# Performance work log

Measured on AMD Instinct MI355X. Metric: run time of the kernel, lower is better.

## Reference

```python
import jax, jax.numpy as jnp
import numpy as np

B, N, T, C = 2, 8192, 32, 64
K, NUM_BASES = 16, 4


def setup_inputs() -> dict:
    key = jax.random.key(0)
    k1, k2, k3, k4, k5 = jax.random.split(key, 5)
    z = jax.random.normal(k1, (B, N, T, C), dtype=jnp.float32)
    neighbor_indices = jax.random.randint(k2, (N, K), 0, N)
    # adjacency initialized as ones + small noise (matches torch init)
    adjacency = jnp.ones((N, K), jnp.float32) + jax.random.normal(k3, (N, K), jnp.float32) * 0.01
    basis_weights = jax.random.normal(k4, (NUM_BASES, N, K), jnp.float32) * 0.02
    channel_coeffs = jax.random.normal(k5, (C, NUM_BASES), jnp.float32)
    return {
        "z": z,
        "neighbor_indices": neighbor_indices,
        "adjacency": adjacency,
        "basis_weights": basis_weights,
        "channel_coeffs": channel_coeffs,
    }


def reference(z, neighbor_indices, adjacency, basis_weights, channel_coeffs):
    # eff_weights: (C, N, K) = einsum over bases ('cb,bnk->cnk' == torch 'ck,knm->cnm')
    eff_weights = jnp.einsum("cb,bnk->cnk", channel_coeffs, basis_weights)
    edge_weights = eff_weights * adjacency[None, :, :]          # (C, N, K)
    z_neigh = z[:, neighbor_indices]                            # (B, N, K, T, C) gather
    # weighted reduction over neighbor axis k, then tanh
    z_out = jnp.einsum("bnktc,cnk->bntc", z_neigh, edge_weights)  # (B, N, T, C)
    return jnp.tanh(z_out)
```

## Files before the change

### kernel.cpp

```cpp
#include <hip/hip_runtime.h>

#define B_ 2
#define N_ 8192
#define T_ 32
#define C_ 64
#define K_ 16
#define NB_ 4

__global__ __launch_bounds__(256) void geodcd_kernel(
    const float* __restrict__ z,
    const int*   __restrict__ nidx,
    const float* __restrict__ adj,
    const float* __restrict__ bw,
    const float* __restrict__ cc,
    float*       __restrict__ out)
{
    const int n   = blockIdx.x;
    const int tid = threadIdx.x;

    __shared__ float ew[K_][C_];
    __shared__ int   idx_s[K_];

    if (tid < K_) idx_s[tid] = nidx[n * K_ + tid];

    for (int i = tid; i < K_ * C_; i += 256) {
        const int k = i >> 6;
        const int c = i & 63;
        float s = 0.f;
#pragma unroll
        for (int b = 0; b < NB_; ++b)
            s += cc[c * NB_ + b] * bw[(b * N_ + n) * K_ + k];
        ew[k][c] = s * adj[n * K_ + k];
    }
    __syncthreads();

    const int c4 = (tid & 15) * 4;
    const int t0 = tid >> 4;

    float4 w[K_];
#pragma unroll
    for (int k = 0; k < K_; ++k)
        w[k] = *(const float4*)&ew[k][c4];

    int zoff[K_];
#pragma unroll
    for (int k = 0; k < K_; ++k)
        zoff[k] = idx_s[k] * (T_ * C_);

#pragma unroll
    for (int b = 0; b < B_; ++b) {
        const float* zb = z   + (size_t)b * (N_ * T_ * C_);
        float*       ob = out + (size_t)b * (N_ * T_ * C_) + n * (T_ * C_);
#pragma unroll
        for (int tt = 0; tt < 2; ++tt) {
            const int t = t0 + tt * 16;
            const int rowoff = t * C_ + c4;
            float4 acc = make_float4(0.f, 0.f, 0.f, 0.f);
#pragma unroll
            for (int k = 0; k < K_; ++k) {
                const float4 v = *(const float4*)&zb[zoff[k] + rowoff];
                acc.x += v.x * w[k].x;
                acc.y += v.y * w[k].y;
                acc.z += v.z * w[k].z;
                acc.w += v.w * w[k].w;
            }
            float4 r;
            r.x = 1.f - 2.f / (__expf(2.f * acc.x) + 1.f);
            r.y = 1.f - 2.f / (__expf(2.f * acc.y) + 1.f);
            r.z = 1.f - 2.f / (__expf(2.f * acc.z) + 1.f);
            r.w = 1.f - 2.f / (__expf(2.f * acc.w) + 1.f);
            *(float4*)&ob[rowoff] = r;
        }
    }
}

extern "C" void kernel_launch(void* const* d_in, const int* in_sizes, int n_in,
                              void* d_out, int out_size, void* d_ws, size_t ws_size,
                              hipStream_t stream) {
    const float* z    = (const float*)d_in[0];
    const int*   nidx = (const int*)  d_in[1];
    const float* adj  = (const float*)d_in[2];
    const float* bw   = (const float*)d_in[3];
    const float* cc   = (const float*)d_in[4];
    float*       out  = (float*)d_out;

    geodcd_kernel<<<N_, 256, 0, stream>>>(z, nidx, adj, bw, cc, out);
}
```

Measured before the change: 491.5 us.

## Retile grid over node groups and (batch, time) slabs with register-computed weights

Each block now handles 16 nodes for one batch and a 2-timestep slab, and the grid's second dimension runs over batch and time chunks. The (C,K) edge weight table is no longer built in shared memory; each thread computes its weights in registers from per-node adj*basis products and the channel coefficients. Stores are nontemporal. The aim is to spread work so that consecutive blocks touch the same time slab of z, improving cache locality for the random gather, and to cut the shared-memory weight setup. The cost is that weight computation is repeated across 32 block rows, and each thread now has fewer loads in flight.

```diff
diff --git a/kernel.cpp b/kernel.cpp
--- a/kernel.cpp
+++ b/kernel.cpp
@@ -7,6 +7,11 @@
 #define K_ 16
 #define NB_ 4
 
+#define NC 16
+#define TC 2
+
+typedef float f4v __attribute__((ext_vector_type(4)));
+
 __global__ __launch_bounds__(256) void geodcd_kernel(
     const float* __restrict__ z,
     const int*   __restrict__ nidx,
@@ -15,63 +20,81 @@
     const float* __restrict__ cc,
     float*       __restrict__ out)
 {
-    const int n   = blockIdx.x;
     const int tid = threadIdx.x;
+    const int n0  = blockIdx.x * NC;
+    const int ph  = blockIdx.y;
+    const int b   = ph >> 4;
+    const int t0  = (ph & 15) * TC;
 
-    __shared__ float ew[K_][C_];
-    __shared__ int   idx_s[K_];
+    __shared__ __align__(16) float qs[NC][K_][NB_];
+    __shared__ int idx_s[NC][K_];
 
-    if (tid < K_) idx_s[tid] = nidx[n * K_ + tid];
-
-    for (int i = tid; i < K_ * C_; i += 256) {
-        const int k = i >> 6;
-        const int c = i & 63;
-        float s = 0.f;
-#pragma unroll
-        for (int b = 0; b < NB_; ++b)
-            s += cc[c * NB_ + b] * bw[(b * N_ + n) * K_ + k];
-        ew[k][c] = s * adj[n * K_ + k];
+    {
+        const int nl = tid >> 4, k = tid & 15;
+        idx_s[nl][k] = nidx[(n0 + nl) * K_ + k];
+    }
+    for (int i = tid; i < NC * K_ * NB_; i += 256) {
+        const int nl = i >> 6;
+        const int k  = (i >> 2) & 15;
+        const int bb = i & 3;
+        qs[nl][k][bb] = adj[(n0 + nl) * K_ + k] * bw[(bb * N_ + (n0 + nl)) * K_ + k];
     }
     __syncthreads();
 
-    const int c4 = (tid & 15) * 4;
-    const int t0 = tid >> 4;
+    const int lane = tid & 15;
+    const int nl   = tid >> 4;
+    const int c4   = lane * 4;
+    const int n    = n0 + nl;
 
-    float4 w[K_];
+    f4v ccv[4];
+#pragma unroll
+    for (int j = 0; j < 4; ++j)
+        ccv[j] = *(const f4v*)&cc[(c4 + j) * NB_];
+
+    f4v w[K_];
+#pragma unroll
+    for (int k = 0; k < K_; ++k) {
+        const f4v q = *(const f4v*)qs[nl][k];
+        f4v wv;
+        wv.x = ccv[0].x * q.x + ccv[0].y * q.y + ccv[0].z * q.z + ccv[0].w * q.w;
+        wv.y = ccv[1].x * q.x + ccv[1].y * q.y + ccv[1].z * q.z + ccv[1].w * q.w;
+        wv.z = ccv[2].x * q.x + ccv[2].y * q.y + ccv[2].z * q.z + ccv[2].w * q.w;
+        wv.w = ccv[3].x * q.x + ccv[3].y * q.y + ccv[3].z * q.z + ccv[3].w * q.w;
+        w[k] = wv;
+    }
+
+    int off[K_];
 #pragma unroll
     for (int k = 0; k < K_; ++k)
-        w[k] = *(const float4*)&ew[k][c4];
+        off[k] = idx_s[nl][k] * (T_ * C_) + t0 * C_ + c4;
 
-    int zoff[K_];
+    const float* zb = z + (size_t)b * (N_ * T_ * C_);
+    f4v a0 = {0.f, 0.f, 0.f, 0.f};
+    f4v a1 = {0.f, 0.f, 0.f, 0.f};
 #pragma unroll
-    for (int k = 0; k < K_; ++k)
-        zoff[k] = idx_s[k] * (T_ * C_);
+    for (int k = 0; k < K_; ++k) {
+        const float* p = zb + off[k];
+        const f4v v0 = *(const f4v*)p;
+        const f4v v1 = *(const f4v*)(p + C_);
+        a0.x += v0.x * w[k].x;  a0.y += v0.y * w[k].y;
+        a0.z += v0.z * w[k].z;  a0.w += v0.w * w[k].w;
+        a1.x += v1.x * w[k].x;  a1.y += v1.y * w[k].y;
+        a1.z += v1.z * w[k].z;  a1.w += v1.w * w[k].w;
+    }
 
-#pragma unroll
-    for (int b = 0; b < B_; ++b) {
-        const float* zb = z   + (size_t)b * (N_ * T_ * C_);
-        float*       ob = out + (size_t)b * (N_ * T_ * C_) + n * (T_ * C_);
-#pragma unroll
-        for (int tt = 0; tt < 2; ++tt) {
-            const int t = t0 + tt * 16;
-            const int rowoff = t * C_ + c4;
-            float4 acc = make_float4(0.f, 0.f, 0.f, 0.f);
-#pragma unroll
-            for (int k = 0; k < K_; ++k) {
-                const float4 v = *(const float4*)&zb[zoff[k] + rowoff];
-                acc.x += v.x * w[k].x;
-                acc.y += v.y * w[k].y;
-                acc.z += v.z * w[k].z;
-                acc.w += v.w * w[k].w;
-            }
-            float4 r;
-            r.x = 1.f - 2.f / (__expf(2.f * acc.x) + 1.f);
-            r.y = 1.f - 2.f / (__expf(2.f * acc.y) + 1.f);
-            r.z = 1.f - 2.f / (__expf(2.f * acc.z) + 1.f);
-            r.w = 1.f - 2.f / (__expf(2.f * acc.w) + 1.f);
-            *(float4*)&ob[rowoff] = r;
-        }
-    }
+    f4v r0, r1;
+    r0.x = 1.f - 2.f / (__expf(2.f * a0.x) + 1.f);
+    r0.y = 1.f - 2.f / (__expf(2.f * a0.y) + 1.f);
+    r0.z = 1.f - 2.f / (__expf(2.f * a0.z) + 1.f);
+    r0.w = 1.f - 2.f / (__expf(2.f * a0.w) + 1.f);
+    r1.x = 1.f - 2.f / (__expf(2.f * a1.x) + 1.f);
+    r1.y = 1.f - 2.f / (__expf(2.f * a1.y) + 1.f);
+    r1.z = 1.f - 2.f / (__expf(2.f * a1.z) + 1.f);
+    r1.w = 1.f - 2.f / (__expf(2.f * a1.w) + 1.f);
+
+    float* ob = out + (((size_t)b * N_ + n) * T_ + t0) * C_ + c4;
+    __builtin_nontemporal_store(r0, (f4v*)ob);
+    __builtin_nontemporal_store(r1, (f4v*)(ob + C_));
 }
 
 extern "C" void kernel_launch(void* const* d_in, const int* in_sizes, int n_in,
@@ -84,5 +107,6 @@
     const float* cc   = (const float*)d_in[4];
     float*       out  = (float*)d_out;
 
-    geodcd_kernel<<<N_, 256, 0, stream>>>(z, nidx, adj, bw, cc, out);
+    dim3 grid(N_ / NC, B_ * (T_ / TC));
+    geodcd_kernel<<<grid, 256, 0, stream>>>(z, nidx, adj, bw, cc, out);
 }
```

Result: slower. 531.5 us (+8.1%).
